# Optimization experiments

Hardware: AMD Instinct MI355X
Metric: run time of the kernel (lower is better)

## Reference

```python
import jax, jax.numpy as jnp
import numpy as np

# Sizes (match init_kwargs config)
B, S, D = 4, 2048, 1024          # batch, seq_len, d_hidden
DE, E, K = 256, 8, 2             # d_expert, n_routed_experts, top_k
N_SHARED = 2
SDE = DE * N_SHARED              # shared expert hidden dim


def silu(v):
    return v * jax.nn.sigmoid(v)


def setup_inputs() -> dict:
    key = jax.random.key(0)
    ks = jax.random.split(key, 9)
    s_d = 1.0 / np.sqrt(D)
    s_de = 1.0 / np.sqrt(DE)
    s_sde = 1.0 / np.sqrt(SDE)
    return {
        "x": jax.random.normal(ks[0], (B, S, D), dtype=jnp.float32),
        "Wg": jax.random.normal(ks[1], (D, E), dtype=jnp.float32) * s_d,          # gate router
        "w_gate": jax.random.normal(ks[2], (E, D, DE), dtype=jnp.float32) * s_d,   # per-expert W_gate
        "w_up": jax.random.normal(ks[3], (E, D, DE), dtype=jnp.float32) * s_d,     # per-expert W_up
        "w_down": jax.random.normal(ks[4], (E, DE, D), dtype=jnp.float32) * s_de,  # per-expert W_down
        "sg": jax.random.normal(ks[5], (D, SDE), dtype=jnp.float32) * s_d,         # shared W_gate
        "su": jax.random.normal(ks[6], (D, SDE), dtype=jnp.float32) * s_d,         # shared W_up
        "sd": jax.random.normal(ks[7], (SDE, D), dtype=jnp.float32) * s_sde,       # shared W_down
        "top_k": K,
    }


def reference(x, Wg, w_gate, w_up, w_down, sg, su, sd, top_k):
    b, s, d = x.shape
    n_exp = Wg.shape[-1]

    # Shared expert (SwiGLU) over all tokens
    shared = (silu(x @ sg) * (x @ su)) @ sd  # [B,S,D]

    # Gating: softmax then top-k (unsorted order irrelevant for weighted sum)
    scores = jax.nn.softmax(x @ Wg, axis=-1)            # [B,S,E]
    topk_scores, topk_ids = jax.lax.top_k(scores, top_k)  # [B,S,K]

    t = b * s
    xf = x.reshape(t, d)
    ts = topk_scores.reshape(t, top_k)
    ti = topk_ids.reshape(t, top_k)

    # Dense combine weights [T,E]: weight of expert e for token t (0 if not routed)
    combine = jnp.zeros((t, n_exp), dtype=x.dtype).at[
        jnp.arange(t)[:, None], ti
    ].add(ts)

    # Per-expert SwiGLU computed densely, combined with routing weights
    g = jnp.einsum('td,edh->teh', xf, w_gate)  # [T,E,DE]
    u = jnp.einsum('td,edh->teh', xf, w_up)    # [T,E,DE]
    h = silu(g) * u
    routed = jnp.einsum('teh,ehd,te->td', h, w_down, combine)  # [T,D]

    return routed.reshape(b, s, d) + shared
```

## Files before the change

### kernel.cpp

```cpp
#include <hip/hip_runtime.h>
#include <stdint.h>

#define TOK   8192
#define DIM   1024
#define NEXP  8
#define TOPK  2
#define WPAD  1028

typedef unsigned short ushort_t;
typedef __attribute__((ext_vector_type(8))) short bf16x8;
typedef __attribute__((ext_vector_type(4))) float f32x4;

__device__ __forceinline__ unsigned short f2bf(float f) {
  unsigned int u = __float_as_uint(f);
  u += 0x7fffu + ((u >> 16) & 1u);
  return (unsigned short)(u >> 16);
}
__device__ __forceinline__ float bf2f(ushort_t u) {
  return __uint_as_float(((unsigned int)u) << 16);
}

__device__ __forceinline__ void gload_lds16(const void* g, void* l) {
  __builtin_amdgcn_global_load_lds(
      (const __attribute__((address_space(1))) void*)(uintptr_t)g,
      (__attribute__((address_space(3))) void*)(unsigned int)(uintptr_t)l,
      16, 0, 0);
}

__global__ __launch_bounds__(256) void k_prep(
    const float* __restrict__ x, const float* __restrict__ Wg,
    ushort_t* __restrict__ xb, int* __restrict__ tid, float* __restrict__ tw,
    const float* __restrict__ sg, const float* __restrict__ su,
    const float* __restrict__ sd, const float* __restrict__ wgm,
    const float* __restrict__ wu, const float* __restrict__ wdn,
    ushort_t* __restrict__ Wsh1, ushort_t* __restrict__ Wsd,
    ushort_t* __restrict__ Wgu, ushort_t* __restrict__ Wd) {
  __shared__ float sm[2 * 64 * 65];
  if (blockIdx.x < 512) {
    for (int j = threadIdx.x; j < DIM * NEXP; j += 256)
      sm[(j & 7) * WPAD + (j >> 3)] = Wg[j];
    __syncthreads();
    const int wid = threadIdx.x >> 6, lane = threadIdx.x & 63;
#pragma unroll
    for (int tt2 = 0; tt2 < 4; ++tt2) {
      const int t = blockIdx.x * 16 + wid * 4 + tt2;
      const float* xr = x + (size_t)t * DIM;
      ushort_t* xw = xb + (size_t)t * DIM;
      float acc[NEXP];
#pragma unroll
      for (int e = 0; e < NEXP; ++e) acc[e] = 0.f;
#pragma unroll
      for (int k = 0; k < 4; ++k) {
        const int i = k * 256 + lane * 4;
        const float4 xv = *(const float4*)(xr + i);
        union { ushort_t u[4]; uint2 v; } s;
        s.u[0] = f2bf(xv.x); s.u[1] = f2bf(xv.y);
        s.u[2] = f2bf(xv.z); s.u[3] = f2bf(xv.w);
        *(uint2*)(xw + i) = s.v;
#pragma unroll
        for (int e = 0; e < NEXP; ++e) {
          const float4 wv = *(const float4*)&sm[e * WPAD + i];
          acc[e] += xv.x * wv.x + xv.y * wv.y + xv.z * wv.z + xv.w * wv.w;
        }
      }
#pragma unroll
      for (int e = 0; e < NEXP; ++e) {
        float v = acc[e];
#pragma unroll
        for (int o = 32; o > 0; o >>= 1) v += __shfl_xor(v, o);
        acc[e] = v;
      }
      if (lane == 0) {
        float mx = acc[0];
#pragma unroll
        for (int e = 1; e < NEXP; ++e) mx = fmaxf(mx, acc[e]);
        float p[NEXP]; float s = 0.f;
#pragma unroll
        for (int e = 0; e < NEXP; ++e) { p[e] = __expf(acc[e] - mx); s += p[e]; }
        const float inv = 1.f / s;
#pragma unroll
        for (int e = 0; e < NEXP; ++e) p[e] *= inv;
        int i1 = 0; float s1 = p[0];
#pragma unroll
        for (int e = 1; e < NEXP; ++e) if (p[e] > s1) { s1 = p[e]; i1 = e; }
        int i2 = -1; float s2 = -1.f;
#pragma unroll
        for (int e = 0; e < NEXP; ++e) if (e != i1 && p[e] > s2) { s2 = p[e]; i2 = e; }
        tid[t * 2] = i1; tid[t * 2 + 1] = i2;
        tw[t * 2] = s1;  tw[t * 2 + 1] = s2;
      }
    }
    return;
  }
  int b = blockIdx.x - 512;
  const float *s0, *s1; ushort_t* dst; int R, C; bool ilv;
  int r0, c0;
  if (b < 128) {
    ilv = true; s0 = sg; s1 = su; dst = Wsh1; R = 1024; C = 512;
    c0 = (b & 7) * 64; r0 = (b >> 3) * 64;
  } else if (b < 640) {
    b -= 128; const int e = b >> 6; b &= 63;
    ilv = true;
    s0 = wgm + (size_t)e * 1024 * 256; s1 = wu + (size_t)e * 1024 * 256;
    dst = Wgu + (size_t)e * 512 * 1024; R = 1024; C = 256;
    c0 = (b & 3) * 64; r0 = (b >> 2) * 64;
  } else if (b < 704) {
    b -= 640; ilv = false; s0 = sd; s1 = sd; dst = Wsd; R = 512; C = 1024;
    c0 = (b & 7) * 128; r0 = (b >> 3) * 64;
  } else {
    b -= 704; const int e = b >> 5; b &= 31;
    ilv = false;
    s0 = wdn + (size_t)e * 256 * 1024; s1 = s0;
    dst = Wd + (size_t)e * 1024 * 256; R = 256; C = 1024;
    c0 = (b & 7) * 128; r0 = (b >> 3) * 64;
  }
  const int row16 = threadIdx.x >> 4;
  const int q16   = threadIdx.x & 15;
#pragma unroll
  for (int p = 0; p < 2; ++p) {
    const float* s = p ? s1 : s0;
    const int cc = ilv ? c0 : (c0 + p * 64);
    float (*tt)[65] = (float(*)[65])(sm + p * 64 * 65);
#pragma unroll
    for (int i = 0; i < 64; i += 16) {
      const float4 v = *(const float4*)&s[(size_t)(r0 + row16 + i) * C + cc + q16 * 4];
      tt[q16 * 4 + 0][row16 + i] = v.x;
      tt[q16 * 4 + 1][row16 + i] = v.y;
      tt[q16 * 4 + 2][row16 + i] = v.z;
      tt[q16 * 4 + 3][row16 + i] = v.w;
    }
  }
  __syncthreads();
#pragma unroll
  for (int p = 0; p < 2; ++p) {
    const int cc = ilv ? c0 : (c0 + p * 64);
    float (*tt)[65] = (float(*)[65])(sm + p * 64 * 65);
#pragma unroll
    for (int i = 0; i < 64; i += 16) {
      const int n = cc + row16 + i;
      const int drow = ilv ? (2 * n + p) : n;
      const float4 v = *(const float4*)&tt[row16 + i][q16 * 4];
      union { ushort_t u[4]; uint2 w; } s4;
      s4.u[0] = f2bf(v.x); s4.u[1] = f2bf(v.y);
      s4.u[2] = f2bf(v.z); s4.u[3] = f2bf(v.w);
      *(uint2*)&dst[(size_t)drow * R + r0 + q16 * 4] = s4.w;
    }
  }
}

__global__ __launch_bounds__(1024) void k_scan(const int* __restrict__ tid,
                                               int* __restrict__ cnt,
                                               int* __restrict__ off,
                                               int* __restrict__ cnt2) {
  __shared__ int h[NEXP];
  if (threadIdx.x < NEXP) h[threadIdx.x] = 0;
  __syncthreads();
  int loc[NEXP];
#pragma unroll
  for (int e = 0; e < NEXP; ++e) loc[e] = 0;
  const int4* t4 = (const int4*)tid;
#pragma unroll
  for (int k = 0; k < TOK * TOPK / 4 / 1024; ++k) {
    const int4 v = t4[threadIdx.x + k * 1024];
#pragma unroll
    for (int e = 0; e < NEXP; ++e)
      loc[e] += (v.x == e) + (v.y == e) + (v.z == e) + (v.w == e);
  }
#pragma unroll
  for (int e = 0; e < NEXP; ++e) if (loc[e]) atomicAdd(&h[e], loc[e]);
  __syncthreads();
  if (threadIdx.x == 0) {
    int run = 0;
    for (int e = 0; e < NEXP; ++e) { off[e] = run; cnt[e] = h[e]; run += h[e]; }
  }
  if (threadIdx.x < NEXP) cnt2[threadIdx.x] = 0;
}

__global__ __launch_bounds__(256) void k_scatter(const int* __restrict__ tid,
                                                 const float* __restrict__ tw,
                                                 const int* __restrict__ off,
                                                 int* __restrict__ cnt2,
                                                 int* __restrict__ tok,
                                                 float* __restrict__ wgt,
                                                 int* __restrict__ dstrow) {
  const int t = blockIdx.x * 256 + threadIdx.x;
  const int lane = threadIdx.x & 63;
#pragma unroll
  for (int j = 0; j < TOPK; ++j) {
    const int e = tid[t * 2 + j];
    const float w = tw[t * 2 + j];
    int slot = 0;
#pragma unroll
    for (int ee = 0; ee < NEXP; ++ee) {
      const unsigned long long m = __ballot(e == ee);
      if (m) {
        const int r = __popcll(m & ((1ull << lane) - 1ull));
        const int leader = __ffsll((unsigned long long)m) - 1;
        int base = 0;
        if (lane == leader) base = atomicAdd(&cnt2[ee], (int)__popcll(m));
        base = __shfl(base, leader);
        if (e == ee) slot = off[ee] + base + r;
      }
    }
    tok[slot] = t;
    wgt[slot] = w;
    dstrow[slot] = t * 2 + j;
  }
}

__global__ __launch_bounds__(256) void k_gemm1(
    const ushort_t* __restrict__ A0, const ushort_t* __restrict__ Bgu,
    const ushort_t* __restrict__ Bsh,
    ushort_t* __restrict__ he, ushort_t* __restrict__ hs,
    const int* __restrict__ tok,
    const int* __restrict__ cnt, const int* __restrict__ off) {
  constexpr int K = 1024, NB = 4, NGROUP = 16, MBSLOT = 16;
  constexpr int NWG = NGROUP * MBSLOT * NB;
  __shared__ __attribute__((aligned(16))) ushort_t lA[2][128 * 64];
  __shared__ __attribute__((aligned(16))) ushort_t lB[2][128 * 64];

  const int wg = (blockIdx.x % 8) * (NWG / 8) + blockIdx.x / 8;
  const int g = wg / (MBSLOT * NB);
  const int rem = wg % (MBSLOT * NB);
  const int mbslot = rem / NB;
  const int nb = rem % NB;
  const int nBase = nb * 128;

  int m_e, offE = 0, rowq = 0, hh = 0;
  bool gat = false;
  const ushort_t* Abase = A0;
  const ushort_t* Bblk;
  if (g < 8) {
    gat = true; m_e = cnt[g]; offE = off[g];
    Bblk = Bgu + (size_t)g * 512 * 1024;
  } else {
    const int q = (g - 8) >> 1; hh = (g - 8) & 1;
    rowq = q * 2048; m_e = 2048;
    Abase = A0 + (size_t)rowq * 1024;
    Bblk = Bsh + (size_t)hh * 512 * 1024;
  }
  if (m_e == 0) return;

  const int wid = threadIdx.x >> 6, lane = threadIdx.x & 63;
  const int wm = wid >> 1, wn = wid & 1;
  const int l15 = lane & 15, lq = lane >> 4;

  const ushort_t* bptr[4];
#pragma unroll
  for (int cc = 0; cc < 4; ++cc) {
    const int c = wid * 4 + cc;
    const int rl = c * 8 + (lane >> 3);
    const int slot = (lane & 7) ^ (rl & 7);
    bptr[cc] = Bblk + (size_t)(nBase + rl) * K + slot * 8;
  }

  for (int mb = mbslot; mb * 128 < m_e; mb += MBSLOT) {
    const int mBase = mb * 128;
    const ushort_t* aptr[4];
#pragma unroll
    for (int cc = 0; cc < 4; ++cc) {
      const int c = wid * 4 + cc;
      const int rl = c * 8 + (lane >> 3);
      const int slot = (lane & 7) ^ (rl & 7);
      const int gr = mBase + rl;
      const int gc = (gr < m_e) ? gr : (m_e - 1);
      const ushort_t* ar;
      if (gat) ar = A0 + (size_t)tok[offE + gc] * 1024;
      else     ar = Abase + (size_t)gc * K;
      aptr[cc] = ar + slot * 8;
    }

    auto stage = [&](int buf, int ktv) {
#pragma unroll
      for (int cc = 0; cc < 4; ++cc) {
        const int c = wid * 4 + cc;
        gload_lds16(aptr[cc] + ktv, &lA[buf][c * 512]);
        gload_lds16(bptr[cc] + ktv, &lB[buf][c * 512]);
      }
    };

    f32x4 acc[4][4];
#pragma unroll
    for (int mi = 0; mi < 4; ++mi)
#pragma unroll
      for (int ni = 0; ni < 4; ++ni) acc[mi][ni] = (f32x4){0.f, 0.f, 0.f, 0.f};

    stage(0, 0);
    int cur = 0;
    for (int kt = 0; kt < K; kt += 64) {
      if (kt + 64 < K) {
        stage(cur ^ 1, kt + 64);
        asm volatile("s_waitcnt vmcnt(8)" ::: "memory");
      } else {
        asm volatile("s_waitcnt vmcnt(0)" ::: "memory");
      }
      __builtin_amdgcn_s_barrier();
#pragma unroll
      for (int kk = 0; kk < 2; ++kk) {
        bf16x8 af[4], bfr[4];
#pragma unroll
        for (int mi = 0; mi < 4; ++mi) {
          const int row = wm * 64 + mi * 16 + l15;
          const int cb = ((kk * 32 + lq * 8) * 2) ^ ((row & 7) << 4);
          af[mi] = *(const bf16x8*)((const char*)lA + cur * 16384 + row * 128 + cb);
        }
#pragma unroll
        for (int ni = 0; ni < 4; ++ni) {
          const int row = wn * 64 + ni * 16 + l15;
          const int cb = ((kk * 32 + lq * 8) * 2) ^ ((row & 7) << 4);
          bfr[ni] = *(const bf16x8*)((const char*)lB + cur * 16384 + row * 128 + cb);
        }
#pragma unroll
        for (int mi = 0; mi < 4; ++mi)
#pragma unroll
          for (int ni = 0; ni < 4; ++ni)
            acc[mi][ni] = __builtin_amdgcn_mfma_f32_16x16x32_bf16(
                af[mi], bfr[ni], acc[mi][ni], 0, 0, 0);
      }
      __builtin_amdgcn_s_barrier();
      cur ^= 1;
    }

#pragma unroll
    for (int mi = 0; mi < 4; ++mi) {
#pragma unroll
      for (int r = 0; r < 4; ++r) {
        const int gg = mBase + wm * 64 + mi * 16 + lq * 4 + r;
        const bool ok = gg < m_e;
#pragma unroll
        for (int ni = 0; ni < 4; ++ni) {
          const float v = acc[mi][ni][r];
          const int c = nBase + wn * 64 + ni * 16 + l15;
          const float o = __shfl_xor(v, 1);
          if (!(c & 1) && ok) {
            const float hv = (v / (1.f + __expf(-v))) * o;
            if (gat) he[(size_t)(offE + gg) * 256 + (c >> 1)] = f2bf(hv);
            else     hs[(size_t)(rowq + gg) * 512 + hh * 256 + (c >> 1)] = f2bf(hv);
          }
        }
      }
    }
  }
}

__global__ __launch_bounds__(512, 1) void k_gemm2r(
    const ushort_t* __restrict__ he, const ushort_t* __restrict__ Wd,
    ushort_t* __restrict__ contrib, const float* __restrict__ wgt,
    const int* __restrict__ cnt, const int* __restrict__ off,
    const int* __restrict__ dstrow) {
  constexpr int K = 256;
  __shared__ __attribute__((aligned(16))) ushort_t lB[128 * 256];
  __shared__ __attribute__((aligned(16))) ushort_t lA[2][256 * 64];

  const int wg = (blockIdx.x & 7) * 32 + (blockIdx.x >> 3);
  const int e = wg >> 5;
  const int r = wg & 31;
  const int nb = r >> 2;
  const int mslot = r & 3;
  const int nBase = nb * 128;

  const int m_e = cnt[e];
  if (m_e == 0) return;
  const int offE = off[e];
  const ushort_t* Abase = he + (size_t)offE * K;
  const ushort_t* Bblk = Wd + (size_t)e * 1024 * K;

  const int wid = threadIdx.x >> 6, lane = threadIdx.x & 63;
  const int wm = wid >> 1, wn = wid & 1;
  const int l15 = lane & 15, lq = lane >> 4;

#pragma unroll
  for (int i = 0; i < 8; ++i) {
    const int sl = (wid * 8 + i) * 64 + lane;
    const int row = sl >> 5;
    const int s = sl & 31;
    const int c = (s & ~7) | ((s & 7) ^ (row & 7));
    gload_lds16(Bblk + (size_t)(nBase + row) * K + c * 8,
                ((char*)lB) + (size_t)(wid * 8 + i) * 1024);
  }

  auto stageA = [&](int buf, int mBase, int h) {
#pragma unroll
    for (int i = 0; i < 4; ++i) {
      const int sl = (wid * 4 + i) * 64 + lane;
      const int row = sl >> 3;
      const int s = sl & 7;
      const int c = s ^ (row & 7);
      const int gr = mBase + row;
      const int gc = (gr < m_e) ? gr : (m_e - 1);
      gload_lds16(Abase + (size_t)gc * K + h * 64 + c * 8,
                  ((char*)lA) + buf * 32768 + (size_t)(wid * 4 + i) * 1024);
    }
  };

  stageA(0, mslot * 256, 0);
  int cur = 0;
  for (int tm = mslot; tm * 256 < m_e; tm += 4) {
    const int mBase = tm * 256;
    f32x4 acc[4][4];
#pragma unroll
    for (int mi = 0; mi < 4; ++mi)
#pragma unroll
      for (int ni = 0; ni < 4; ++ni) acc[mi][ni] = (f32x4){0.f, 0.f, 0.f, 0.f};

    for (int h = 0; h < 4; ++h) {
      int nh = h + 1, ntm = tm;
      if (nh == 4) { nh = 0; ntm = tm + 4; }
      const bool has_next = (ntm * 256 < m_e);
      if (has_next) {
        stageA(cur ^ 1, ntm * 256, nh);
        asm volatile("s_waitcnt vmcnt(4)" ::: "memory");
      } else {
        asm volatile("s_waitcnt vmcnt(0)" ::: "memory");
      }
      __builtin_amdgcn_s_barrier();
      const char* sA = (const char*)lA + cur * 32768;
#pragma unroll
      for (int kk = 0; kk < 2; ++kk) {
        bf16x8 af[4], bfr[4];
#pragma unroll
        for (int mi = 0; mi < 4; ++mi) {
          const int row = wm * 64 + mi * 16 + l15;
          const int cb = ((kk * 4 + lq) ^ (row & 7)) << 4;
          af[mi] = *(const bf16x8*)(sA + row * 128 + cb);
        }
#pragma unroll
        for (int ni = 0; ni < 4; ++ni) {
          const int brow = wn * 64 + ni * 16 + l15;
          const int ck = h * 8 + kk * 4 + lq;
          const int s = (ck & ~7) | ((ck & 7) ^ (brow & 7));
          bfr[ni] = *(const bf16x8*)((const char*)lB + brow * 512 + s * 16);
        }
#pragma unroll
        for (int mi = 0; mi < 4; ++mi)
#pragma unroll
          for (int ni = 0; ni < 4; ++ni)
            acc[mi][ni] = __builtin_amdgcn_mfma_f32_16x16x32_bf16(
                af[mi], bfr[ni], acc[mi][ni], 0, 0, 0);
      }
      __builtin_amdgcn_s_barrier();
      cur ^= 1;
    }

#pragma unroll
    for (int mi = 0; mi < 4; ++mi) {
#pragma unroll
      for (int rr = 0; rr < 4; ++rr) {
        const int gg = mBase + wm * 64 + mi * 16 + lq * 4 + rr;
        if (gg < m_e) {
          const float w = wgt[offE + gg];
          const int dr = dstrow[offE + gg];
#pragma unroll
          for (int ni = 0; ni < 4; ++ni) {
            const int c = nBase + wn * 64 + ni * 16 + l15;
            contrib[(size_t)dr * 1024 + c] = f2bf(acc[mi][ni][rr] * w);
          }
        }
      }
    }
  }
  asm volatile("s_waitcnt vmcnt(0)" ::: "memory");
}

__global__ __launch_bounds__(512, 1) void k_gemm2s(
    const ushort_t* __restrict__ hs, const ushort_t* __restrict__ Wsd,
    const ushort_t* __restrict__ contrib, float* __restrict__ out) {
  constexpr int K = 512;
  __shared__ __attribute__((aligned(16))) ushort_t lB[64 * 512];
  __shared__ __attribute__((aligned(16))) ushort_t lA[2][256 * 64];

  const int wg = (blockIdx.x & 7) * 32 + (blockIdx.x >> 3);
  const int nstrip = wg >> 4;
  const int mslot = wg & 15;
  const int nBase = nstrip * 64;

  const int wid = threadIdx.x >> 6, lane = threadIdx.x & 63;
  const int wm = wid >> 1, wn = wid & 1;
  const int l15 = lane & 15, lq = lane >> 4;

#pragma unroll
  for (int i = 0; i < 8; ++i) {
    const int sl = (wid * 8 + i) * 64 + lane;
    const int row = sl >> 6;
    const int s = sl & 63;
    const int c = (s & ~7) | ((s & 7) ^ (row & 7));
    gload_lds16(Wsd + (size_t)(nBase + row) * K + c * 8,
                ((char*)lB) + (size_t)(wid * 8 + i) * 1024);
  }

  auto stageA = [&](int buf, int mBase, int h) {
#pragma unroll
    for (int i = 0; i < 4; ++i) {
      const int sl = (wid * 4 + i) * 64 + lane;
      const int row = sl >> 3;
      const int s = sl & 7;
      const int c = s ^ (row & 7);
      gload_lds16(hs + (size_t)(mBase + row) * K + h * 64 + c * 8,
                  ((char*)lA) + buf * 32768 + (size_t)(wid * 4 + i) * 1024);
    }
  };

  stageA(0, mslot * 256, 0);
  int cur = 0;
  for (int tm = mslot; tm * 256 < TOK; tm += 16) {
    const int mBase = tm * 256;
    f32x4 acc[4][2];
#pragma unroll
    for (int mi = 0; mi < 4; ++mi)
#pragma unroll
      for (int ni = 0; ni < 2; ++ni) acc[mi][ni] = (f32x4){0.f, 0.f, 0.f, 0.f};

    for (int h = 0; h < 8; ++h) {
      int nh = h + 1, ntm = tm;
      if (nh == 8) { nh = 0; ntm = tm + 16; }
      const bool has_next = (ntm * 256 < TOK);
      if (has_next) {
        stageA(cur ^ 1, ntm * 256, nh);
        asm volatile("s_waitcnt vmcnt(4)" ::: "memory");
      } else {
        asm volatile("s_waitcnt vmcnt(0)" ::: "memory");
      }
      __builtin_amdgcn_s_barrier();
      const char* sA = (const char*)lA + cur * 32768;
#pragma unroll
      for (int kk = 0; kk < 2; ++kk) {
        bf16x8 af[4], bfr[2];
#pragma unroll
        for (int mi = 0; mi < 4; ++mi) {
          const int row = wm * 64 + mi * 16 + l15;
          const int cb = ((kk * 4 + lq) ^ (row & 7)) << 4;
          af[mi] = *(const bf16x8*)(sA + row * 128 + cb);
        }
#pragma unroll
        for (int ni = 0; ni < 2; ++ni) {
          const int brow = wn * 32 + ni * 16 + l15;
          const int ck = h * 8 + kk * 4 + lq;
          const int s = (ck & ~7) | ((ck & 7) ^ (brow & 7));
          bfr[ni] = *(const bf16x8*)((const char*)lB + brow * 1024 + s * 16);
        }
#pragma unroll
        for (int mi = 0; mi < 4; ++mi)
#pragma unroll
          for (int ni = 0; ni < 2; ++ni)
            acc[mi][ni] = __builtin_amdgcn_mfma_f32_16x16x32_bf16(
                af[mi], bfr[ni], acc[mi][ni], 0, 0, 0);
      }
      __builtin_amdgcn_s_barrier();
      cur ^= 1;
    }

#pragma unroll
    for (int mi = 0; mi < 4; ++mi) {
#pragma unroll
      for (int rr = 0; rr < 4; ++rr) {
        const int gg = mBase + wm * 64 + mi * 16 + lq * 4 + rr;
#pragma unroll
        for (int ni = 0; ni < 2; ++ni) {
          const int c = nBase + wn * 32 + ni * 16 + l15;
          out[(size_t)gg * 1024 + c] = acc[mi][ni][rr]
              + bf2f(contrib[(size_t)(gg * 2) * 1024 + c])
              + bf2f(contrib[(size_t)(gg * 2 + 1) * 1024 + c]);
        }
      }
    }
  }
  asm volatile("s_waitcnt vmcnt(0)" ::: "memory");
}

extern "C" void kernel_launch(void* const* d_in, const int* in_sizes, int n_in,
                              void* d_out, int out_size, void* d_ws, size_t ws_size,
                              hipStream_t stream) {
  (void)in_sizes; (void)n_in; (void)out_size; (void)ws_size;
  const float* x      = (const float*)d_in[0];
  const float* Wg     = (const float*)d_in[1];
  const float* w_gate = (const float*)d_in[2];
  const float* w_up   = (const float*)d_in[3];
  const float* w_down = (const float*)d_in[4];
  const float* sg     = (const float*)d_in[5];
  const float* su     = (const float*)d_in[6];
  const float* sd     = (const float*)d_in[7];
  float* out = (float*)d_out;

  char* ws = (char*)d_ws;
  size_t o = 0;
  ushort_t* xb    = (ushort_t*)(ws + o); o += (size_t)TOK * DIM * 2;
  ushort_t* Wsh1  = (ushort_t*)(ws + o); o += (size_t)1024 * 1024 * 2;
  ushort_t* Wsd   = (ushort_t*)(ws + o); o += (size_t)1024 * 512 * 2;
  ushort_t* Wgu   = (ushort_t*)(ws + o); o += (size_t)NEXP * 512 * 1024 * 2;
  ushort_t* Wd    = (ushort_t*)(ws + o); o += (size_t)NEXP * 1024 * 256 * 2;
  ushort_t* hs    = (ushort_t*)(ws + o); o += (size_t)TOK * 512 * 2;
  ushort_t* he    = (ushort_t*)(ws + o); o += (size_t)TOK * TOPK * 256 * 2;
  int*   tid   = (int*)(ws + o);   o += (size_t)TOK * TOPK * 4;
  float* tw    = (float*)(ws + o); o += (size_t)TOK * TOPK * 4;
  int*   tok   = (int*)(ws + o);   o += (size_t)TOK * TOPK * 4;
  float* wgt   = (float*)(ws + o); o += (size_t)TOK * TOPK * 4;
  int*   dstrow= (int*)(ws + o);   o += (size_t)TOK * TOPK * 4;
  int*   cnt   = (int*)(ws + o);   o += 64;
  int*   offp  = (int*)(ws + o);   o += 64;
  int*   cnt2  = (int*)(ws + o);   o += 64;
  ushort_t* contrib = (ushort_t*)(ws + o);

  k_prep<<<1472, 256, 0, stream>>>(x, Wg, xb, tid, tw, sg, su, sd,
                                   w_gate, w_up, w_down, Wsh1, Wsd, Wgu, Wd);
  k_scan<<<1, 1024, 0, stream>>>(tid, cnt, offp, cnt2);
  k_scatter<<<TOK / 256, 256, 0, stream>>>(tid, tw, offp, cnt2, tok, wgt, dstrow);

  k_gemm1<<<1024, 256, 0, stream>>>(xb, Wgu, Wsh1, he, hs, tok, cnt, offp);
  k_gemm2r<<<256, 512, 0, stream>>>(he, Wd, contrib, wgt, cnt, offp, dstrow);
  k_gemm2s<<<256, 512, 0, stream>>>(hs, Wsd, contrib, out);
}
```

Measured before the change: 177.3 us.

## Retile gate/up GEMM to 256x256 tiles with 4-stage pipelined LDS loads

Rewrites the first grouped GEMM to use 512-thread workgroups computing 256x256 tiles with BK=32 and a four-buffer async global-to-LDS pipeline, one barrier per k-step, and MFMA priority boosting. The grid becomes a persistent 256 blocks, with the work split remapped between routed experts and the shared expert. The goal is more data reuse per LDS load, fewer barriers and better overlap of memory loads with MFMA work. The trade-off is higher register pressure (32 accumulators per wave) and possible load imbalance, since a routed expert with few tokens leaves its blocks idle.

Result: slower. 197.3 us (+11.3%).

```diff
diff --git a/kernel.cpp b/kernel.cpp
--- a/kernel.cpp
+++ b/kernel.cpp
@@ -208,124 +208,112 @@
   }
 }
 
-__global__ __launch_bounds__(256) void k_gemm1(
+__global__ __launch_bounds__(512, 1) void k_gemm1(
     const ushort_t* __restrict__ A0, const ushort_t* __restrict__ Bgu,
     const ushort_t* __restrict__ Bsh,
     ushort_t* __restrict__ he, ushort_t* __restrict__ hs,
     const int* __restrict__ tok,
     const int* __restrict__ cnt, const int* __restrict__ off) {
-  constexpr int K = 1024, NB = 4, NGROUP = 16, MBSLOT = 16;
-  constexpr int NWG = NGROUP * MBSLOT * NB;
-  __shared__ __attribute__((aligned(16))) ushort_t lA[2][128 * 64];
-  __shared__ __attribute__((aligned(16))) ushort_t lB[2][128 * 64];
-
-  const int wg = (blockIdx.x % 8) * (NWG / 8) + blockIdx.x / 8;
-  const int g = wg / (MBSLOT * NB);
-  const int rem = wg % (MBSLOT * NB);
-  const int mbslot = rem / NB;
-  const int nb = rem % NB;
-  const int nBase = nb * 128;
-
-  int m_e, offE = 0, rowq = 0, hh = 0;
-  bool gat = false;
-  const ushort_t* Abase = A0;
+  constexpr int K = 1024, NT = 32;
+  __shared__ __attribute__((aligned(16))) ushort_t lA[4][256 * 32];
+  __shared__ __attribute__((aligned(16))) ushort_t lB[4][256 * 32];
+
+  const int wg = (blockIdx.x & 7) * 32 + (blockIdx.x >> 3);
+  int mbslot, nb, MB, m_e, offE = 0;
+  bool gat;
   const ushort_t* Bblk;
-  if (g < 8) {
+  if (wg < 128) {
+    const int g = wg >> 4;
+    const int r = wg & 15;
+    mbslot = r >> 1; nb = r & 1; MB = 8;
     gat = true; m_e = cnt[g]; offE = off[g];
     Bblk = Bgu + (size_t)g * 512 * 1024;
   } else {
-    const int q = (g - 8) >> 1; hh = (g - 8) & 1;
-    rowq = q * 2048; m_e = 2048;
-    Abase = A0 + (size_t)rowq * 1024;
-    Bblk = Bsh + (size_t)hh * 512 * 1024;
+    const int r = wg - 128;
+    mbslot = r >> 2; nb = r & 3; MB = 32;
+    gat = false; m_e = TOK;
+    Bblk = Bsh;
   }
   if (m_e == 0) return;
+  const int nBase = nb * 256;
 
   const int wid = threadIdx.x >> 6, lane = threadIdx.x & 63;
-  const int wm = wid >> 1, wn = wid & 1;
+  const int wm = wid >> 2, wn = wid & 3;
   const int l15 = lane & 15, lq = lane >> 4;
 
-  const ushort_t* bptr[4];
-#pragma unroll
-  for (int cc = 0; cc < 4; ++cc) {
-    const int c = wid * 4 + cc;
-    const int rl = c * 8 + (lane >> 3);
-    const int slot = (lane & 7) ^ (rl & 7);
-    bptr[cc] = Bblk + (size_t)(nBase + rl) * K + slot * 8;
-  }
-
-  for (int mb = mbslot; mb * 128 < m_e; mb += MBSLOT) {
-    const int mBase = mb * 128;
-    const ushort_t* aptr[4];
-#pragma unroll
-    for (int cc = 0; cc < 4; ++cc) {
-      const int c = wid * 4 + cc;
-      const int rl = c * 8 + (lane >> 3);
-      const int slot = (lane & 7) ^ (rl & 7);
-      const int gr = mBase + rl;
+  int srow[2], scol[2];
+  const ushort_t* bsrc[2];
+#pragma unroll
+  for (int c = 0; c < 2; ++c) {
+    const int sl = (c * 8 + wid) * 64 + lane;
+    srow[c] = sl >> 2;
+    scol[c] = (sl & 3) ^ ((srow[c] >> 1) & 3);
+    bsrc[c] = Bblk + (size_t)(nBase + srow[c]) * K + scol[c] * 8;
+  }
+
+  for (int mb = mbslot; mb * 256 < m_e; mb += MB) {
+    const int mBase = mb * 256;
+    const ushort_t* asrc[2];
+#pragma unroll
+    for (int c = 0; c < 2; ++c) {
+      const int gr = mBase + srow[c];
       const int gc = (gr < m_e) ? gr : (m_e - 1);
-      const ushort_t* ar;
-      if (gat) ar = A0 + (size_t)tok[offE + gc] * 1024;
-      else     ar = Abase + (size_t)gc * K;
-      aptr[cc] = ar + slot * 8;
-    }
-
-    auto stage = [&](int buf, int ktv) {
-#pragma unroll
-      for (int cc = 0; cc < 4; ++cc) {
-        const int c = wid * 4 + cc;
-        gload_lds16(aptr[cc] + ktv, &lA[buf][c * 512]);
-        gload_lds16(bptr[cc] + ktv, &lB[buf][c * 512]);
+      const ushort_t* ar = gat ? (A0 + (size_t)tok[offE + gc] * 1024)
+                               : (A0 + (size_t)gc * K);
+      asrc[c] = ar + scol[c] * 8;
+    }
+
+    auto stage = [&](int buf, int kt) {
+#pragma unroll
+      for (int c = 0; c < 2; ++c) {
+        gload_lds16(asrc[c] + kt, &lA[buf][(c * 8 + wid) * 512]);
+        gload_lds16(bsrc[c] + kt, &lB[buf][(c * 8 + wid) * 512]);
       }
     };
 
-    f32x4 acc[4][4];
-#pragma unroll
-    for (int mi = 0; mi < 4; ++mi)
+    f32x4 acc[8][4];
+#pragma unroll
+    for (int mi = 0; mi < 8; ++mi)
 #pragma unroll
       for (int ni = 0; ni < 4; ++ni) acc[mi][ni] = (f32x4){0.f, 0.f, 0.f, 0.f};
 
-    stage(0, 0);
-    int cur = 0;
-    for (int kt = 0; kt < K; kt += 64) {
-      if (kt + 64 < K) {
-        stage(cur ^ 1, kt + 64);
-        asm volatile("s_waitcnt vmcnt(8)" ::: "memory");
-      } else {
-        asm volatile("s_waitcnt vmcnt(0)" ::: "memory");
-      }
+    stage(0, 0); stage(1, 32); stage(2, 64);
+    for (int t = 0; t < NT; ++t) {
+      if (t + 2 < NT)      asm volatile("s_waitcnt vmcnt(8)" ::: "memory");
+      else if (t + 1 < NT) asm volatile("s_waitcnt vmcnt(4)" ::: "memory");
+      else                 asm volatile("s_waitcnt vmcnt(0)" ::: "memory");
       __builtin_amdgcn_s_barrier();
-#pragma unroll
-      for (int kk = 0; kk < 2; ++kk) {
-        bf16x8 af[4], bfr[4];
-#pragma unroll
-        for (int mi = 0; mi < 4; ++mi) {
-          const int row = wm * 64 + mi * 16 + l15;
-          const int cb = ((kk * 32 + lq * 8) * 2) ^ ((row & 7) << 4);
-          af[mi] = *(const bf16x8*)((const char*)lA + cur * 16384 + row * 128 + cb);
-        }
-#pragma unroll
-        for (int ni = 0; ni < 4; ++ni) {
-          const int row = wn * 64 + ni * 16 + l15;
-          const int cb = ((kk * 32 + lq * 8) * 2) ^ ((row & 7) << 4);
-          bfr[ni] = *(const bf16x8*)((const char*)lB + cur * 16384 + row * 128 + cb);
-        }
-#pragma unroll
-        for (int mi = 0; mi < 4; ++mi)
-#pragma unroll
-          for (int ni = 0; ni < 4; ++ni)
-            acc[mi][ni] = __builtin_amdgcn_mfma_f32_16x16x32_bf16(
-                af[mi], bfr[ni], acc[mi][ni], 0, 0, 0);
-      }
-      __builtin_amdgcn_s_barrier();
-      cur ^= 1;
-    }
-
-#pragma unroll
-    for (int mi = 0; mi < 4; ++mi) {
+      if (t + 3 < NT) stage((t + 3) & 3, (t + 3) * 32);
+
+      const char* sA = (const char*)lA[t & 3];
+      const char* sB = (const char*)lB[t & 3];
+      bf16x8 af[8], bfr[4];
+#pragma unroll
+      for (int ni = 0; ni < 4; ++ni) {
+        const int row = wn * 64 + ni * 16 + l15;
+        bfr[ni] = *(const bf16x8*)(sB + row * 64 + ((lq ^ ((row >> 1) & 3)) << 4));
+      }
+#pragma unroll
+      for (int mi = 0; mi < 8; ++mi) {
+        const int row = wm * 128 + mi * 16 + l15;
+        af[mi] = *(const bf16x8*)(sA + row * 64 + ((lq ^ ((row >> 1) & 3)) << 4));
+      }
+      __builtin_amdgcn_s_setprio(1);
+#pragma unroll
+      for (int mi = 0; mi < 8; ++mi)
+#pragma unroll
+        for (int ni = 0; ni < 4; ++ni)
+          acc[mi][ni] = __builtin_amdgcn_mfma_f32_16x16x32_bf16(
+              af[mi], bfr[ni], acc[mi][ni], 0, 0, 0);
+      __builtin_amdgcn_s_setprio(0);
+    }
+    __builtin_amdgcn_s_barrier();
+
+#pragma unroll
+    for (int mi = 0; mi < 8; ++mi) {
 #pragma unroll
       for (int r = 0; r < 4; ++r) {
-        const int gg = mBase + wm * 64 + mi * 16 + lq * 4 + r;
+        const int gg = mBase + wm * 128 + mi * 16 + lq * 4 + r;
         const bool ok = gg < m_e;
 #pragma unroll
         for (int ni = 0; ni < 4; ++ni) {
@@ -335,7 +323,7 @@
           if (!(c & 1) && ok) {
             const float hv = (v / (1.f + __expf(-v))) * o;
             if (gat) he[(size_t)(offE + gg) * 256 + (c >> 1)] = f2bf(hv);
-            else     hs[(size_t)(rowq + gg) * 512 + hh * 256 + (c >> 1)] = f2bf(hv);
+            else     hs[(size_t)gg * 512 + (c >> 1)] = f2bf(hv);
           }
         }
       }
@@ -605,7 +593,7 @@
   k_scan<<<1, 1024, 0, stream>>>(tid, cnt, offp, cnt2);
   k_scatter<<<TOK / 256, 256, 0, stream>>>(tid, tw, offp, cnt2, tok, wgt, dstrow);
 
-  k_gemm1<<<1024, 256, 0, stream>>>(xb, Wgu, Wsh1, he, hs, tok, cnt, offp);
+  k_gemm1<<<256, 512, 0, stream>>>(xb, Wgu, Wsh1, he, hs, tok, cnt, offp);
   k_gemm2r<<<256, 512, 0, stream>>>(he, Wd, contrib, wgt, cnt, offp, dstrow);
   k_gemm2s<<<256, 512, 0, stream>>>(hs, Wsd, contrib, out);
 }
```

## Give each wave private A-staging buffers in down-proj GEMMs, drop block barriers

Applied to the files above, without the earlier changes.

Both down-projection GEMMs (routed and shared) now give every wave its own 32-row A tile in private double-buffered LDS. Each wave covers the full N width of the block, so the per-k-step workgroup barriers go away and each wave waits only on its own loads. The routed kernel also changes its block-to-expert mapping and lets blocks with no work return early after the initial barrier. The B-tile LDS swizzle is widened to a full-row XOR. The cost is that each wave now reads more B fragments from LDS per A fragment, which lowers data reuse in registers.

Measured after the change: 171.4 us. -3.4%, faster.

```diff
diff --git a/kernel.cpp b/kernel.cpp
--- a/kernel.cpp
+++ b/kernel.cpp
@@ -350,114 +350,115 @@
     const int* __restrict__ dstrow) {
   constexpr int K = 256;
   __shared__ __attribute__((aligned(16))) ushort_t lB[128 * 256];
-  __shared__ __attribute__((aligned(16))) ushort_t lA[2][256 * 64];
-
-  const int wg = (blockIdx.x & 7) * 32 + (blockIdx.x >> 3);
-  const int e = wg >> 5;
-  const int r = wg & 31;
-  const int nb = r >> 2;
-  const int mslot = r & 3;
+  __shared__ __attribute__((aligned(16))) ushort_t lA[8][2][32 * 64];
+
+  const int e = blockIdx.x & 7;
+  const int c0 = blockIdx.x >> 3;
+  const int nb = c0 & 7;
+  const int mslot = c0 >> 3;
   const int nBase = nb * 128;
 
   const int m_e = cnt[e];
-  if (m_e == 0) return;
-  const int offE = off[e];
+  const int offE = (m_e > 0) ? off[e] : 0;
   const ushort_t* Abase = he + (size_t)offE * K;
   const ushort_t* Bblk = Wd + (size_t)e * 1024 * K;
 
   const int wid = threadIdx.x >> 6, lane = threadIdx.x & 63;
-  const int wm = wid >> 1, wn = wid & 1;
   const int l15 = lane & 15, lq = lane >> 4;
 
-#pragma unroll
-  for (int i = 0; i < 8; ++i) {
-    const int sl = (wid * 8 + i) * 64 + lane;
-    const int row = sl >> 5;
-    const int s = sl & 31;
-    const int c = (s & ~7) | ((s & 7) ^ (row & 7));
-    gload_lds16(Bblk + (size_t)(nBase + row) * K + c * 8,
-                ((char*)lB) + (size_t)(wid * 8 + i) * 1024);
-  }
-
-  auto stageA = [&](int buf, int mBase, int h) {
+  if (m_e > 0) {
+#pragma unroll
+    for (int i = 0; i < 8; ++i) {
+      const int L = (wid * 8 + i) * 64 + lane;
+      const int row = L >> 5, s = L & 31;
+      const int ss = s ^ (row & 31);
+      gload_lds16(Bblk + (size_t)(nBase + row) * K + ss * 8,
+                  ((char*)lB) + (size_t)(wid * 8 + i) * 1024);
+    }
+  }
+
+  char* lAw = (char*)&lA[wid][0][0];
+  auto stageA = [&](int buf, int chunk, int kc) {
 #pragma unroll
     for (int i = 0; i < 4; ++i) {
-      const int sl = (wid * 4 + i) * 64 + lane;
-      const int row = sl >> 3;
-      const int s = sl & 7;
-      const int c = s ^ (row & 7);
-      const int gr = mBase + row;
-      const int gc = (gr < m_e) ? gr : (m_e - 1);
-      gload_lds16(Abase + (size_t)gc * K + h * 64 + c * 8,
-                  ((char*)lA) + buf * 32768 + (size_t)(wid * 4 + i) * 1024);
+      const int L = i * 64 + lane;
+      const int row = L >> 3, s = L & 7;
+      const int ss = s ^ (row & 7);
+      int gr = chunk * 32 + row;
+      if (gr >= m_e) gr = m_e - 1;
+      gload_lds16(Abase + (size_t)gr * K + kc * 64 + ss * 8,
+                  lAw + (size_t)buf * 4096 + (size_t)i * 1024);
     }
   };
 
-  stageA(0, mslot * 256, 0);
-  int cur = 0;
-  for (int tm = mslot; tm * 256 < m_e; tm += 4) {
-    const int mBase = tm * 256;
-    f32x4 acc[4][4];
-#pragma unroll
-    for (int mi = 0; mi < 4; ++mi)
-#pragma unroll
-      for (int ni = 0; ni < 4; ++ni) acc[mi][ni] = (f32x4){0.f, 0.f, 0.f, 0.f};
-
-    for (int h = 0; h < 4; ++h) {
-      int nh = h + 1, ntm = tm;
-      if (nh == 4) { nh = 0; ntm = tm + 4; }
-      const bool has_next = (ntm * 256 < m_e);
-      if (has_next) {
-        stageA(cur ^ 1, ntm * 256, nh);
+  int cw = mslot * 8 + wid;
+  bool active = (m_e > 0) && (cw * 32 < m_e);
+  if (m_e > 0) stageA(0, active ? cw : 0, 0);
+  asm volatile("s_waitcnt vmcnt(4)" ::: "memory");
+  __builtin_amdgcn_s_barrier();
+  if (!active) return;
+
+  int buf = 0;
+  while (active) {
+    f32x4 acc[2][8];
+#pragma unroll
+    for (int mi = 0; mi < 2; ++mi)
+#pragma unroll
+      for (int ni = 0; ni < 8; ++ni) acc[mi][ni] = (f32x4){0.f, 0.f, 0.f, 0.f};
+
+    for (int kc = 0; kc < 4; ++kc) {
+      int nc = cw, nk = kc + 1;
+      if (nk == 4) { nk = 0; nc = cw + 32; }
+      if (nc * 32 < m_e) {
+        stageA(buf ^ 1, nc, nk);
         asm volatile("s_waitcnt vmcnt(4)" ::: "memory");
       } else {
         asm volatile("s_waitcnt vmcnt(0)" ::: "memory");
       }
-      __builtin_amdgcn_s_barrier();
-      const char* sA = (const char*)lA + cur * 32768;
+      const char* sA = lAw + buf * 4096;
 #pragma unroll
       for (int kk = 0; kk < 2; ++kk) {
-        bf16x8 af[4], bfr[4];
-#pragma unroll
-        for (int mi = 0; mi < 4; ++mi) {
-          const int row = wm * 64 + mi * 16 + l15;
-          const int cb = ((kk * 4 + lq) ^ (row & 7)) << 4;
-          af[mi] = *(const bf16x8*)(sA + row * 128 + cb);
-        }
-#pragma unroll
-        for (int ni = 0; ni < 4; ++ni) {
-          const int brow = wn * 64 + ni * 16 + l15;
-          const int ck = h * 8 + kk * 4 + lq;
-          const int s = (ck & ~7) | ((ck & 7) ^ (brow & 7));
-          bfr[ni] = *(const bf16x8*)((const char*)lB + brow * 512 + s * 16);
-        }
-#pragma unroll
-        for (int mi = 0; mi < 4; ++mi)
-#pragma unroll
-          for (int ni = 0; ni < 4; ++ni)
+        bf16x8 af[2], bfr[8];
+#pragma unroll
+        for (int mi = 0; mi < 2; ++mi) {
+          const int row = mi * 16 + l15;
+          af[mi] = *(const bf16x8*)(sA + row * 128 + (((kk * 4 + lq) ^ (row & 7)) << 4));
+        }
+#pragma unroll
+        for (int ni = 0; ni < 8; ++ni) {
+          const int brow = ni * 16 + l15;
+          const int ck = kc * 8 + kk * 4 + lq;
+          bfr[ni] = *(const bf16x8*)((const char*)lB + brow * 512 +
+                                     ((ck ^ (brow & 31)) << 4));
+        }
+#pragma unroll
+        for (int mi = 0; mi < 2; ++mi)
+#pragma unroll
+          for (int ni = 0; ni < 8; ++ni)
             acc[mi][ni] = __builtin_amdgcn_mfma_f32_16x16x32_bf16(
                 af[mi], bfr[ni], acc[mi][ni], 0, 0, 0);
       }
-      __builtin_amdgcn_s_barrier();
-      cur ^= 1;
-    }
-
-#pragma unroll
-    for (int mi = 0; mi < 4; ++mi) {
-#pragma unroll
-      for (int rr = 0; rr < 4; ++rr) {
-        const int gg = mBase + wm * 64 + mi * 16 + lq * 4 + rr;
+      buf ^= 1;
+    }
+
+#pragma unroll
+    for (int mi = 0; mi < 2; ++mi) {
+#pragma unroll
+      for (int r = 0; r < 4; ++r) {
+        const int gg = cw * 32 + mi * 16 + lq * 4 + r;
         if (gg < m_e) {
           const float w = wgt[offE + gg];
           const int dr = dstrow[offE + gg];
 #pragma unroll
-          for (int ni = 0; ni < 4; ++ni) {
-            const int c = nBase + wn * 64 + ni * 16 + l15;
-            contrib[(size_t)dr * 1024 + c] = f2bf(acc[mi][ni][rr] * w);
+          for (int ni = 0; ni < 8; ++ni) {
+            const int c = nBase + ni * 16 + l15;
+            contrib[(size_t)dr * 1024 + c] = f2bf(acc[mi][ni][r] * w);
           }
         }
       }
     }
+    cw += 32;
+    active = cw * 32 < m_e;
   }
   asm volatile("s_waitcnt vmcnt(0)" ::: "memory");
 }
@@ -467,7 +468,7 @@
     const ushort_t* __restrict__ contrib, float* __restrict__ out) {
   constexpr int K = 512;
   __shared__ __attribute__((aligned(16))) ushort_t lB[64 * 512];
-  __shared__ __attribute__((aligned(16))) ushort_t lA[2][256 * 64];
+  __shared__ __attribute__((aligned(16))) ushort_t lA[8][2][32 * 64];
 
   const int wg = (blockIdx.x & 7) * 32 + (blockIdx.x >> 3);
   const int nstrip = wg >> 4;
@@ -475,94 +476,92 @@
   const int nBase = nstrip * 64;
 
   const int wid = threadIdx.x >> 6, lane = threadIdx.x & 63;
-  const int wm = wid >> 1, wn = wid & 1;
   const int l15 = lane & 15, lq = lane >> 4;
 
 #pragma unroll
   for (int i = 0; i < 8; ++i) {
-    const int sl = (wid * 8 + i) * 64 + lane;
-    const int row = sl >> 6;
-    const int s = sl & 63;
-    const int c = (s & ~7) | ((s & 7) ^ (row & 7));
-    gload_lds16(Wsd + (size_t)(nBase + row) * K + c * 8,
+    const int L = (wid * 8 + i) * 64 + lane;
+    const int row = L >> 6, s = L & 63;
+    const int ss = s ^ row;
+    gload_lds16(Wsd + (size_t)(nBase + row) * K + ss * 8,
                 ((char*)lB) + (size_t)(wid * 8 + i) * 1024);
   }
 
-  auto stageA = [&](int buf, int mBase, int h) {
+  char* lAw = (char*)&lA[wid][0][0];
+  auto stageA = [&](int buf, int chunk, int kc) {
 #pragma unroll
     for (int i = 0; i < 4; ++i) {
-      const int sl = (wid * 4 + i) * 64 + lane;
-      const int row = sl >> 3;
-      const int s = sl & 7;
-      const int c = s ^ (row & 7);
-      gload_lds16(hs + (size_t)(mBase + row) * K + h * 64 + c * 8,
-                  ((char*)lA) + buf * 32768 + (size_t)(wid * 4 + i) * 1024);
+      const int L = i * 64 + lane;
+      const int row = L >> 3, s = L & 7;
+      const int ss = s ^ (row & 7);
+      gload_lds16(hs + (size_t)(chunk * 32 + row) * K + kc * 64 + ss * 8,
+                  lAw + (size_t)buf * 4096 + (size_t)i * 1024);
     }
   };
 
-  stageA(0, mslot * 256, 0);
-  int cur = 0;
-  for (int tm = mslot; tm * 256 < TOK; tm += 16) {
-    const int mBase = tm * 256;
-    f32x4 acc[4][2];
-#pragma unroll
-    for (int mi = 0; mi < 4; ++mi)
-#pragma unroll
-      for (int ni = 0; ni < 2; ++ni) acc[mi][ni] = (f32x4){0.f, 0.f, 0.f, 0.f};
-
-    for (int h = 0; h < 8; ++h) {
-      int nh = h + 1, ntm = tm;
-      if (nh == 8) { nh = 0; ntm = tm + 16; }
-      const bool has_next = (ntm * 256 < TOK);
-      if (has_next) {
-        stageA(cur ^ 1, ntm * 256, nh);
+  int cw = mslot * 8 + wid;
+  stageA(0, cw, 0);
+  asm volatile("s_waitcnt vmcnt(4)" ::: "memory");
+  __builtin_amdgcn_s_barrier();
+
+  int buf = 0;
+  for (int rep = 0; rep < 2; ++rep) {
+    f32x4 acc[2][4];
+#pragma unroll
+    for (int mi = 0; mi < 2; ++mi)
+#pragma unroll
+      for (int ni = 0; ni < 4; ++ni) acc[mi][ni] = (f32x4){0.f, 0.f, 0.f, 0.f};
+
+    for (int kc = 0; kc < 8; ++kc) {
+      int nc = cw, nk = kc + 1;
+      if (nk == 8) { nk = 0; nc = cw + 128; }
+      if (nc < 256) {
+        stageA(buf ^ 1, nc, nk);
         asm volatile("s_waitcnt vmcnt(4)" ::: "memory");
       } else {
         asm volatile("s_waitcnt vmcnt(0)" ::: "memory");
       }
-      __builtin_amdgcn_s_barrier();
-      const char* sA = (const char*)lA + cur * 32768;
+      const char* sA = lAw + buf * 4096;
 #pragma unroll
       for (int kk = 0; kk < 2; ++kk) {
-        bf16x8 af[4], bfr[2];
-#pragma unroll
-        for (int mi = 0; mi < 4; ++mi) {
-          const int row = wm * 64 + mi * 16 + l15;
-          const int cb = ((kk * 4 + lq) ^ (row & 7)) << 4;
-          af[mi] = *(const bf16x8*)(sA + row * 128 + cb);
-        }
-#pragma unroll
-        for (int ni = 0; ni < 2; ++ni) {
-          const int brow = wn * 32 + ni * 16 + l15;
-          const int ck = h * 8 + kk * 4 + lq;
-          const int s = (ck & ~7) | ((ck & 7) ^ (brow & 7));
-          bfr[ni] = *(const bf16x8*)((const char*)lB + brow * 1024 + s * 16);
-        }
-#pragma unroll
-        for (int mi = 0; mi < 4; ++mi)
-#pragma unroll
-          for (int ni = 0; ni < 2; ++ni)
+        bf16x8 af[2], bfr[4];
+#pragma unroll
+        for (int mi = 0; mi < 2; ++mi) {
+          const int row = mi * 16 + l15;
+          af[mi] = *(const bf16x8*)(sA + row * 128 + (((kk * 4 + lq) ^ (row & 7)) << 4));
+        }
+#pragma unroll
+        for (int ni = 0; ni < 4; ++ni) {
+          const int brow = ni * 16 + l15;
+          const int ck = kc * 8 + kk * 4 + lq;
+          bfr[ni] = *(const bf16x8*)((const char*)lB + brow * 1024 +
+                                     ((ck ^ brow) << 4));
+        }
+#pragma unroll
+        for (int mi = 0; mi < 2; ++mi)
+#pragma unroll
+          for (int ni = 0; ni < 4; ++ni)
             acc[mi][ni] = __builtin_amdgcn_mfma_f32_16x16x32_bf16(
                 af[mi], bfr[ni], acc[mi][ni], 0, 0, 0);
       }
-      __builtin_amdgcn_s_barrier();
-      cur ^= 1;
-    }
-
-#pragma unroll
-    for (int mi = 0; mi < 4; ++mi) {
-#pragma unroll
-      for (int rr = 0; rr < 4; ++rr) {
-        const int gg = mBase + wm * 64 + mi * 16 + lq * 4 + rr;
-#pragma unroll
-        for (int ni = 0; ni < 2; ++ni) {
-          const int c = nBase + wn * 32 + ni * 16 + l15;
-          out[(size_t)gg * 1024 + c] = acc[mi][ni][rr]
+      buf ^= 1;
+    }
+
+#pragma unroll
+    for (int mi = 0; mi < 2; ++mi) {
+#pragma unroll
+      for (int r = 0; r < 4; ++r) {
+        const int gg = cw * 32 + mi * 16 + lq * 4 + r;
+#pragma unroll
+        for (int ni = 0; ni < 4; ++ni) {
+          const int c = nBase + ni * 16 + l15;
+          out[(size_t)gg * 1024 + c] = acc[mi][ni][r]
               + bf2f(contrib[(size_t)(gg * 2) * 1024 + c])
               + bf2f(contrib[(size_t)(gg * 2 + 1) * 1024 + c]);
         }
       }
     }
+    cw += 128;
   }
   asm volatile("s_waitcnt vmcnt(0)" ::: "memory");
 }
```
